# Optimization experiments

Hardware: AMD Instinct MI355X
Metric: run time of the kernel (lower is better)

Reference implementation:

```python
import jax, jax.numpy as jnp
import numpy as np

WS = 7          # window size (square)
HEADS = 8
HEAD_DIM = 32
SCALE = HEAD_DIM ** -0.5

def _relative_indices():
    # static [49,49,2] indices into the (2*WS-1)^2 bias table, values in [0, 2*WS-2]
    idx = np.array([[x, y] for x in range(WS) for y in range(WS)])  # [49,2]
    rel = idx[None, :, :] - idx[:, None, :]                          # [49,49,2], in [-6,6]
    rel = rel - rel.min()                                            # shift to [0,12]
    return rel

_REL = _relative_indices()

def setup_inputs() -> dict:
    key = jax.random.key(0)
    ks = jax.random.split(key, 5)
    dim, inner = 256, HEADS * HEAD_DIM
    return {
        "x": jax.random.normal(ks[0], (32, 56, 56, dim), dtype=jnp.float32),
        "w_qkv": jax.random.normal(ks[1], (dim, 3 * inner), dtype=jnp.float32) * (dim ** -0.5),
        "w_out": jax.random.normal(ks[2], (inner, dim), dtype=jnp.float32) * (inner ** -0.5),
        "b_out": jax.random.normal(ks[3], (dim,), dtype=jnp.float32) * 0.01,
        "pos_emb": jax.random.normal(ks[4], (2 * WS - 1, 2 * WS - 1), dtype=jnp.float32),
    }

def _to_windows(t):
    # [b, nwh*WS, nww*WS, heads*d] -> [b, heads, nwh*nww, WS*WS, d]
    b, H, W, _ = t.shape
    nwh, nww = H // WS, W // WS
    t = t.reshape(b, nwh, WS, nww, WS, HEADS, HEAD_DIM)
    t = t.transpose(0, 5, 1, 3, 2, 4, 6)  # b h nwh nww wh ww d
    return t.reshape(b, HEADS, nwh * nww, WS * WS, HEAD_DIM)

def reference(x, w_qkv, w_out, b_out, pos_emb):
    b, H, W, _ = x.shape
    nwh, nww = H // WS, W // WS
    qkv = x @ w_qkv                                  # [b,H,W,3*inner]
    q, k, v = jnp.split(qkv, 3, axis=-1)
    q, k, v = _to_windows(q), _to_windows(k), _to_windows(v)  # [b,h,w,49,d]
    dots = jnp.einsum('bhwid,bhwjd->bhwij', q, k) * SCALE      # [b,h,w,49,49]
    bias = pos_emb[_REL[:, :, 0], _REL[:, :, 1]]               # gathered [49,49]
    attn = jax.nn.softmax(dots + bias, axis=-1)
    out = jnp.einsum('bhwij,bhwjd->bhwid', attn, v)            # [b,h,w,49,d]
    out = out.reshape(b, HEADS, nwh, nww, WS, WS, HEAD_DIM)
    out = out.transpose(0, 2, 4, 3, 5, 1, 6)                   # b nwh wh nww ww h d
    out = out.reshape(b, H, W, HEADS * HEAD_DIM)
    return out @ w_out + b_out
```

## Files before the change

kernel.cpp:

```cpp
#include <hip/hip_runtime.h>
#include <hip/hip_bf16.h>
#include <stdint.h>

typedef __attribute__((ext_vector_type(8))) short bf16x8;
typedef __attribute__((ext_vector_type(4))) float f32x4;
typedef __attribute__((ext_vector_type(16))) float f32x16;

#define AS1(p) ((const __attribute__((address_space(1))) void*)(p))
#define AS3(p) ((__attribute__((address_space(3))) void*)(p))

static __device__ __forceinline__ unsigned short f2bf(float f) {
  union { float f; unsigned u; } v; v.f = f;
  unsigned r = v.u + 0x7fffu + ((v.u >> 16) & 1u);
  return (unsigned short)(r >> 16);
}
static __device__ __forceinline__ float f4get(float4 v, int r) {
  return r == 0 ? v.x : r == 1 ? v.y : r == 2 ? v.z : v.w;
}
static __device__ __forceinline__ int grow(int rowbase, int t) {
  return rowbase + (t / 7) * 56 + (t % 7);
}

__global__ __launch_bounds__(256) void cast_x_kernel(const float* __restrict__ x,
                                                     unsigned short* __restrict__ xb,
                                                     int n4) {
  int idx = blockIdx.x * 256 + threadIdx.x;
  int stride = gridDim.x * 256;
  for (int i = idx; i < n4; i += stride) {
    float4 v = ((const float4*)x)[i];
    ushort4 o;
    o.x = f2bf(v.x); o.y = f2bf(v.y); o.z = f2bf(v.z); o.w = f2bf(v.w);
    ((ushort4*)xb)[i] = o;
  }
}

__global__ __launch_bounds__(256) void prep_w_kernel(const float* __restrict__ wqkv,
                                                     const float* __restrict__ wout,
                                                     unsigned short* __restrict__ wqkvT,
                                                     unsigned short* __restrict__ woutT) {
  int id = blockIdx.x * 256 + threadIdx.x;
  if (id < 768 * 256) {
    int n = id >> 8, k = id & 255;
    float v = wqkv[k * 768 + n];
    if (n < 256) v *= 0.17677669529663687f;
    wqkvT[id] = f2bf(v);
  } else {
    int id2 = id - 768 * 256;
    int n = id2 >> 8, k = id2 & 255;
    woutT[id2] = f2bf(wout[k * 256 + n]);
  }
}

template <int N_COLS, bool OUT_F32, bool BIAS>
__global__ __launch_bounds__(256) void gemm_kernel(const unsigned short* __restrict__ A,
                                                   const unsigned short* __restrict__ Bt,
                                                   void* __restrict__ Cout,
                                                   const float* __restrict__ bias) {
  constexpr int K = 256;
  constexpr int NB = N_COLS / 128;
  __shared__ __align__(16) unsigned short lA[128 * 64];
  __shared__ __align__(16) unsigned short lB[128 * 64];
  const int tid = threadIdx.x;
  const int lane = tid & 63;
  const int wid = tid >> 6;
  const int wr = wid >> 1, wc = wid & 1;

  const int orig = blockIdx.x;
  const int cpx = gridDim.x >> 3;
  const int swz = (orig & 7) * cpx + (orig >> 3);
  const int m0 = (swz / NB) * 128;
  const int n0 = (swz % NB) * 128;

  f32x4 acc[4][4];
#pragma unroll
  for (int i = 0; i < 4; ++i)
#pragma unroll
    for (int j = 0; j < 4; ++j) acc[i][j] = (f32x4){0.f, 0.f, 0.f, 0.f};

  for (int k0 = 0; k0 < K; k0 += 64) {
#pragma unroll
    for (int i = 0; i < 4; ++i) {
      int cidx = i * 256 + tid;
      int r = cidx >> 3, cc = cidx & 7;
      int scc = cc ^ (r & 7);
      const unsigned short* g = A + (size_t)(m0 + r) * K + k0 + scc * 8;
      __builtin_amdgcn_global_load_lds(AS1(g), AS3(&lA[cidx * 8]), 16, 0, 0);
    }
#pragma unroll
    for (int i = 0; i < 4; ++i) {
      int cidx = i * 256 + tid;
      int r = cidx >> 3, cc = cidx & 7;
      int scc = cc ^ (r & 7);
      const unsigned short* g = Bt + (size_t)(n0 + r) * K + k0 + scc * 8;
      __builtin_amdgcn_global_load_lds(AS1(g), AS3(&lB[cidx * 8]), 16, 0, 0);
    }
    __syncthreads();
#pragma unroll
    for (int kk = 0; kk < 2; ++kk) {
      bf16x8 af[4], bfr[4];
#pragma unroll
      for (int mi = 0; mi < 4; ++mi) {
        int r = wr * 64 + mi * 16 + (lane & 15);
        int kc = kk * 4 + (lane >> 4);
        int pc = kc ^ (r & 7);
        af[mi] = *reinterpret_cast<const bf16x8*>(&lA[r * 64 + pc * 8]);
      }
#pragma unroll
      for (int ni = 0; ni < 4; ++ni) {
        int r = wc * 64 + ni * 16 + (lane & 15);
        int kc = kk * 4 + (lane >> 4);
        int pc = kc ^ (r & 7);
        bfr[ni] = *reinterpret_cast<const bf16x8*>(&lB[r * 64 + pc * 8]);
      }
#pragma unroll
      for (int mi = 0; mi < 4; ++mi)
#pragma unroll
        for (int ni = 0; ni < 4; ++ni)
          acc[mi][ni] = __builtin_amdgcn_mfma_f32_16x16x32_bf16(af[mi], bfr[ni],
                                                                acc[mi][ni], 0, 0, 0);
    }
    __syncthreads();
  }

  const int rif = (lane >> 4) * 4;
  const int cif = lane & 15;
#pragma unroll
  for (int mi = 0; mi < 4; ++mi) {
#pragma unroll
    for (int ni = 0; ni < 4; ++ni) {
      int col = n0 + wc * 64 + ni * 16 + cif;
      float bv = BIAS ? bias[col] : 0.f;
#pragma unroll
      for (int j = 0; j < 4; ++j) {
        int row = m0 + wr * 64 + mi * 16 + rif + j;
        float v = acc[mi][ni][j] + bv;
        if (OUT_F32)
          ((float*)Cout)[(size_t)row * N_COLS + col] = v;
        else
          ((unsigned short*)Cout)[(size_t)row * N_COLS + col] = f2bf(v);
      }
    }
  }
}

__global__ __launch_bounds__(512) void attn_mfma_kernel(const unsigned short* __restrict__ qkv,
                                                        const float* __restrict__ pe,
                                                        unsigned short* __restrict__ aout) {
  __shared__ float biasL[64 * 64];
  __shared__ unsigned short Vt[8][32 * 72];
  const int tid = threadIdx.x;

  for (int id = tid; id < 4096; id += 512) {
    int i = id >> 6, j = id & 63;
    float v = 0.f;
    if (i < 49 && j < 49) {
      int xi = i / 7, yi = i % 7, xj = j / 7, yj = j % 7;
      v = pe[(xj - xi + 6) * 13 + (yj - yi + 6)];
    }
    biasL[i * 64 + ((((unsigned)j >> 2) ^ (i & 15)) << 2) + (j & 3)] = v;
  }
  __syncthreads();

  const int lane = tid & 63;
  const int wv = tid >> 6;
  const int hi = lane >> 5;
  const int l31 = lane & 31;
  const int h = wv;
  const int win = blockIdx.x;
  const int rowbase = (win >> 6) * 3136 + ((win & 63) >> 3) * 392 + (win & 7) * 7;
  unsigned short* vt = Vt[wv];

  const int vrow = lane < 49 ? lane : 48;
  const unsigned short* vpr = qkv + (size_t)grow(rowbase, vrow) * 768 + h * 32 + 512;
  bf16x8 vr[4];
#pragma unroll
  for (int t = 0; t < 4; ++t) vr[t] = *(const bf16x8*)(vpr + t * 8);
  if (lane >= 49) {
#pragma unroll
    for (int t = 0; t < 4; ++t) vr[t] = bf16x8{0, 0, 0, 0, 0, 0, 0, 0};
  }

  bf16x8 qf[2][2], kf[2][2];
#pragma unroll
  for (int t = 0; t < 2; ++t) {
    int r = t * 32 + l31; if (r > 48) r = 48;
    const unsigned short* base = qkv + (size_t)grow(rowbase, r) * 768 + h * 32;
#pragma unroll
    for (int ks = 0; ks < 2; ++ks) {
      qf[t][ks] = *(const bf16x8*)(base + ks * 16 + hi * 8);
      kf[t][ks] = *(const bf16x8*)(base + 256 + ks * 16 + hi * 8);
    }
  }

  f32x16 acc[2][2];
#pragma unroll
  for (int mi = 0; mi < 2; ++mi)
#pragma unroll
    for (int ni = 0; ni < 2; ++ni) {
#pragma unroll
      for (int z = 0; z < 16; ++z) acc[mi][ni][z] = 0.f;
#pragma unroll
      for (int ks = 0; ks < 2; ++ks)
        acc[mi][ni] = __builtin_amdgcn_mfma_f32_32x32x16_bf16(kf[mi][ks], qf[ni][ks],
                                                              acc[mi][ni], 0, 0, 0);
    }

#pragma unroll
  for (int t = 0; t < 4; ++t)
#pragma unroll
    for (int e = 0; e < 8; ++e)
      vt[(t * 8 + e) * 72 + lane] = (unsigned short)vr[t][e];

  unsigned int pkw[2][2][4][2];
#pragma unroll
  for (int ni = 0; ni < 2; ++ni) {
    const int i = ni * 32 + l31;
    float s[32];
    float m = -3e38f;
#pragma unroll
    for (int mi = 0; mi < 2; ++mi)
#pragma unroll
      for (int q = 0; q < 4; ++q) {
        int cc = (mi * 8 + q * 2 + hi) ^ (i & 15);
        float4 b4 = *(const float4*)&biasL[i * 64 + cc * 4];
#pragma unroll
        for (int r = 0; r < 4; ++r) {
          float v = acc[mi][ni][q * 4 + r] + f4get(b4, r);
          s[mi * 16 + q * 4 + r] = v;
          int j0 = mi * 32 + q * 8 + r;
          if (j0 + 4 * hi < 49) m = fmaxf(m, v);
        }
      }
    m = fmaxf(m, __shfl_xor(m, 32, 64));
    float sum = 0.f;
#pragma unroll
    for (int mi = 0; mi < 2; ++mi)
#pragma unroll
      for (int q = 0; q < 4; ++q)
#pragma unroll
        for (int r = 0; r < 4; ++r) {
          int j0 = mi * 32 + q * 8 + r;
          int idx = mi * 16 + q * 4 + r;
          float e = (j0 + 4 * hi < 49) ? __expf(s[idx] - m) : 0.f;
          s[idx] = e;
          sum += e;
        }
    sum += __shfl_xor(sum, 32, 64);
    float inv = 1.f / sum;
#pragma unroll
    for (int mi = 0; mi < 2; ++mi)
#pragma unroll
      for (int q = 0; q < 4; ++q)
#pragma unroll
        for (int w = 0; w < 2; ++w) {
          float lo = s[mi * 16 + q * 4 + 2 * w] * inv;
          float hp = s[mi * 16 + q * 4 + 2 * w + 1] * inv;
          unsigned int d;
          asm("v_cvt_pk_bf16_f32 %0, %1, %2" : "=v"(d) : "v"(lo), "v"(hp));
          pkw[ni][mi][q][w] = d;
        }
  }

  bf16x8 vfr[4];
#pragma unroll
  for (int ks = 0; ks < 4; ++ks)
    vfr[ks] = *(const bf16x8*)&vt[l31 * 72 + ks * 16 + hi * 8];

  f32x16 oacc[2];
#pragma unroll
  for (int oi = 0; oi < 2; ++oi) {
#pragma unroll
    for (int z = 0; z < 16; ++z) oacc[oi][z] = 0.f;
#pragma unroll
    for (int ks = 0; ks < 4; ++ks) {
      unsigned int a0 = pkw[oi][ks >> 1][(ks & 1) * 2][0];
      unsigned int a1 = pkw[oi][ks >> 1][(ks & 1) * 2][1];
      unsigned int b0 = pkw[oi][ks >> 1][(ks & 1) * 2 + 1][0];
      unsigned int b1 = pkw[oi][ks >> 1][(ks & 1) * 2 + 1][1];
      asm("v_permlane32_swap_b32 %0, %1" : "+v"(a0), "+v"(b0));
      asm("v_permlane32_swap_b32 %0, %1" : "+v"(a1), "+v"(b1));
      union { unsigned int u[4]; bf16x8 v; } pf;
      pf.u[0] = a0; pf.u[1] = a1; pf.u[2] = b0; pf.u[3] = b1;
      oacc[oi] = __builtin_amdgcn_mfma_f32_32x32x16_bf16(pf.v, vfr[ks], oacc[oi], 0, 0, 0);
    }
  }

#pragma unroll
  for (int oi = 0; oi < 2; ++oi)
#pragma unroll
    for (int reg = 0; reg < 16; ++reg) {
      int i = oi * 32 + (reg & 3) + 8 * (reg >> 2) + 4 * hi;
      if (i < 49)
        aout[(size_t)grow(rowbase, i) * 256 + h * 32 + l31] = f2bf(oacc[oi][reg]);
    }
}

extern "C" void kernel_launch(void* const* d_in, const int* in_sizes, int n_in,
                              void* d_out, int out_size, void* d_ws, size_t ws_size,
                              hipStream_t stream) {
  const float* x       = (const float*)d_in[0];
  const float* w_qkv   = (const float*)d_in[1];
  const float* w_out   = (const float*)d_in[2];
  const float* b_out   = (const float*)d_in[3];
  const float* pos_emb = (const float*)d_in[4];
  float* out = (float*)d_out;

  const int M = 32 * 56 * 56;
  char* ws = (char*)d_ws;
  unsigned short* xb    = (unsigned short*)ws;
  unsigned short* qkv   = (unsigned short*)(ws + 51380224);
  unsigned short* aout  = (unsigned short*)(ws + 51380224 + 154140672);
  unsigned short* wqkvT = (unsigned short*)(ws + 256901120);
  unsigned short* woutT = (unsigned short*)(ws + 257294336);

  cast_x_kernel<<<dim3(2048), dim3(256), 0, stream>>>(x, xb, M * 256 / 4);
  prep_w_kernel<<<dim3(1024), dim3(256), 0, stream>>>(w_qkv, w_out, wqkvT, woutT);
  gemm_kernel<768, false, false><<<dim3((M / 128) * 6), dim3(256), 0, stream>>>(xb, wqkvT, qkv, nullptr);
  attn_mfma_kernel<<<dim3(2048), dim3(512), 0, stream>>>(qkv, pos_emb, aout);
  gemm_kernel<256, true, true><<<dim3((M / 128) * 2), dim3(256), 0, stream>>>(aout, woutT, out, b_out);
}
```

Measured before the change: 319.9 us.

## Fuse output projection GEMM into windowed attention kernel

The attention kernel now stages each window's 49x256 bf16 output in shared memory (reusing the V transpose buffer with an XOR swizzle) and multiplies it by the transposed output weights with MFMA, adding the bias and writing fp32 results directly. This removes the separate output-projection GEMM launch and the global round trip of the intermediate attention output. In exchange, each block reloads woutT from global/L2 per window, rows are padded from 49 to 64 so some MFMA work is wasted, and an extra barrier is added.

```diff
diff --git a/kernel.cpp b/kernel.cpp
--- a/kernel.cpp
+++ b/kernel.cpp
@@ -145,9 +145,12 @@
 
 __global__ __launch_bounds__(512) void attn_mfma_kernel(const unsigned short* __restrict__ qkv,
                                                         const float* __restrict__ pe,
-                                                        unsigned short* __restrict__ aout) {
+                                                        const unsigned short* __restrict__ woutT,
+                                                        const float* __restrict__ b_out,
+                                                        float* __restrict__ out) {
   __shared__ float biasL[64 * 64];
   __shared__ unsigned short Vt[8][32 * 72];
+  unsigned short* Olds = &Vt[0][0];
   const int tid = threadIdx.x;
 
   for (int id = tid; id < 4096; id += 512) {
@@ -265,6 +268,8 @@
 #pragma unroll
   for (int ks = 0; ks < 4; ++ks)
     vfr[ks] = *(const bf16x8*)&vt[l31 * 72 + ks * 16 + hi * 8];
+
+  __syncthreads();
 
   f32x16 oacc[2];
 #pragma unroll
@@ -285,13 +290,46 @@
     }
   }
 
-#pragma unroll
-  for (int oi = 0; oi < 2; ++oi)
+  {
+    const int dg = h * 32 + l31;
+    const int c = dg >> 3;
+#pragma unroll
+    for (int oi = 0; oi < 2; ++oi)
+#pragma unroll
+      for (int reg = 0; reg < 16; ++reg) {
+        int i = oi * 32 + (reg & 3) + 8 * (reg >> 2) + 4 * hi;
+        int pc = (c & 24) | ((c ^ i) & 7);
+        Olds[i * 256 + pc * 8 + (dg & 7)] = f2bf(oacc[oi][reg]);
+      }
+  }
+  __syncthreads();
+
+  const float bias_v = b_out[wv * 32 + l31];
+  f32x16 cacc[2];
+#pragma unroll
+  for (int t = 0; t < 2; ++t)
+#pragma unroll
+    for (int z = 0; z < 16; ++z) cacc[t][z] = 0.f;
+  const unsigned short* wrow = woutT + (size_t)(wv * 32 + l31) * 256;
+#pragma unroll
+  for (int ks = 0; ks < 16; ++ks) {
+    bf16x8 bf = *(const bf16x8*)(wrow + ks * 16 + hi * 8);
+#pragma unroll
+    for (int t = 0; t < 2; ++t) {
+      int row = t * 32 + l31;
+      int c = ks * 2 + hi;
+      int pc = (c & 24) | ((c ^ row) & 7);
+      bf16x8 af = *(const bf16x8*)&Olds[row * 256 + pc * 8];
+      cacc[t] = __builtin_amdgcn_mfma_f32_32x32x16_bf16(af, bf, cacc[t], 0, 0, 0);
+    }
+  }
+#pragma unroll
+  for (int t = 0; t < 2; ++t)
 #pragma unroll
     for (int reg = 0; reg < 16; ++reg) {
-      int i = oi * 32 + (reg & 3) + 8 * (reg >> 2) + 4 * hi;
+      int i = t * 32 + (reg & 3) + 8 * (reg >> 2) + 4 * hi;
       if (i < 49)
-        aout[(size_t)grow(rowbase, i) * 256 + h * 32 + l31] = f2bf(oacc[oi][reg]);
+        out[(size_t)grow(rowbase, i) * 256 + wv * 32 + l31] = cacc[t][reg] + bias_v;
     }
 }
 
@@ -309,13 +347,11 @@
   char* ws = (char*)d_ws;
   unsigned short* xb    = (unsigned short*)ws;
   unsigned short* qkv   = (unsigned short*)(ws + 51380224);
-  unsigned short* aout  = (unsigned short*)(ws + 51380224 + 154140672);
-  unsigned short* wqkvT = (unsigned short*)(ws + 256901120);
-  unsigned short* woutT = (unsigned short*)(ws + 257294336);
+  unsigned short* wqkvT = (unsigned short*)(ws + 205520896);
+  unsigned short* woutT = (unsigned short*)(ws + 205914112);
 
   cast_x_kernel<<<dim3(2048), dim3(256), 0, stream>>>(x, xb, M * 256 / 4);
   prep_w_kernel<<<dim3(1024), dim3(256), 0, stream>>>(w_qkv, w_out, wqkvT, woutT);
   gemm_kernel<768, false, false><<<dim3((M / 128) * 6), dim3(256), 0, stream>>>(xb, wqkvT, qkv, nullptr);
-  attn_mfma_kernel<<<dim3(2048), dim3(512), 0, stream>>>(qkv, pos_emb, aout);
-  gemm_kernel<256, true, true><<<dim3((M / 128) * 2), dim3(256), 0, stream>>>(aout, woutT, out, b_out);
-}
+  attn_mfma_kernel<<<dim3(2048), dim3(512), 0, stream>>>(qkv, pos_emb, woutT, b_out, out);
+}
```

After: 334.2 us. +4.5%, slower.
